# Optimization experiments

Hardware: AMD Instinct MI355X
Metric: run time of the kernel (lower is better)

The kernel has to match this reference:

```python
import jax, jax.numpy as jnp
import numpy as np

N, E, B = 4096, 12288, 64
CLIP, HID, H = 768, 1024, 4
PREFIX, MBART = 4, 768
C2 = PREFIX * MBART
NEG_SLOPE = 0.2


def setup_inputs() -> dict:
    key = jax.random.key(0)
    ks = jax.random.split(key, 30)
    s = 0.05

    def nrm(k, shape, sc=s):
        return jax.random.normal(k, shape, dtype=jnp.float32) * sc

    inp = {
        "x": nrm(ks[0], (N, CLIP), 1.0),
        "edge_index": jax.random.randint(ks[1], (2, E), 0, N),
        "edge_attr": nrm(ks[2], (E, CLIP), 1.0),
        "batch": jnp.sort(jax.random.randint(ks[3], (N,), 0, B)),
        # GATConv 1 (clip_dim -> hidden, H heads, concat=False)
        "W1": nrm(ks[4], (CLIP, H, HID)),
        "att_src1": nrm(ks[5], (H, HID)),
        "att_dst1": nrm(ks[6], (H, HID)),
        "W_edge1": nrm(ks[7], (CLIP, H, HID)),
        "att_edge1": nrm(ks[8], (H, HID)),
        "bias1": jnp.zeros((HID,), jnp.float32),
        "prelu1": jnp.float32(0.25),
        # GATConv 2 (hidden -> prefix*mbart, H heads, concat=False)
        "W2": nrm(ks[9], (HID, H, C2)),
        "att_src2": nrm(ks[10], (H, C2)),
        "att_dst2": nrm(ks[11], (H, C2)),
        "W_edge2": nrm(ks[12], (CLIP, H, C2)),
        "att_edge2": nrm(ks[13], (H, C2)),
        "bias2": jnp.zeros((C2,), jnp.float32),
        "prelu2": jnp.float32(0.25),
        # AttentionalAggregation gate_nn: Linear/PReLU/Linear/PReLU/Linear
        "gW1": nrm(ks[14], (C2, HID)),
        "gb1": jnp.zeros((HID,), jnp.float32),
        "ga1": jnp.float32(0.25),
        "gW2": nrm(ks[15], (HID, HID)),
        "gb2": jnp.zeros((HID,), jnp.float32),
        "ga2": jnp.float32(0.25),
        "gW3": nrm(ks[16], (HID, 1)),
        "gb3": jnp.zeros((1,), jnp.float32),
    }
    return inp


def _prelu(x, a):
    return jnp.where(x >= 0, x, a * x)


def _gat_conv(x, src, dst, edge_attr, W, att_s, att_d, W_e, att_e, bias, n):
    # PyG GATConv, concat=False: shared lin for src/dst, edge-attention term,
    # leaky_relu, segment softmax over destination neighborhoods, scatter-add.
    xl = jnp.einsum('nd,dhc->nhc', x, W)                  # [N,H,C]
    a_s = jnp.einsum('nhc,hc->nh', xl, att_s)             # [N,H]
    a_d = jnp.einsum('nhc,hc->nh', xl, att_d)             # [N,H]
    # fuse lin_edge + att_edge: alpha_e = edge_attr @ (W_e . att_e)
    w_e = jnp.einsum('dhc,hc->dh', W_e, att_e)            # [D_edge,H]
    a_e = edge_attr @ w_e                                 # [E,H]
    alpha = jax.nn.leaky_relu(a_s[src] + a_d[dst] + a_e, NEG_SLOPE)
    # segment softmax grouped by dst
    amax = jax.ops.segment_max(alpha, dst, num_segments=n)
    amax = jnp.where(jnp.isfinite(amax), amax, 0.0)
    ex = jnp.exp(alpha - amax[dst])
    den = jax.ops.segment_sum(ex, dst, num_segments=n)
    coef = ex / (den[dst] + 1e-16)                        # [E,H]
    msg = coef[:, :, None] * xl[src]                      # [E,H,C]
    out = jax.ops.segment_sum(msg, dst, num_segments=n)   # [N,H,C]
    return out.mean(axis=1) + bias                        # concat=False -> head mean


def _forward(x, edge_index, edge_attr, batch,
             W1, att_src1, att_dst1, W_edge1, att_edge1, bias1, prelu1,
             W2, att_src2, att_dst2, W_edge2, att_edge2, bias2, prelu2,
             gW1, gb1, ga1, gW2, gb2, ga2, gW3, gb3):
    n = x.shape[0]
    src, dst = edge_index[0], edge_index[1]
    # add_self_loops with fill_value='mean': self-loop edge_attr = mean of
    # incoming edge_attr per destination node (0 if isolated)
    ones = jnp.ones((src.shape[0],), x.dtype)
    deg = jax.ops.segment_sum(ones, dst, num_segments=n)
    mean_attr = jax.ops.segment_sum(edge_attr, dst, num_segments=n) / jnp.clip(deg, 1.0)[:, None]
    loops = jnp.arange(n)
    src_a = jnp.concatenate([src, loops])
    dst_a = jnp.concatenate([dst, loops])
    ea = jnp.concatenate([edge_attr, mean_attr], axis=0)

    h = _gat_conv(x, src_a, dst_a, ea, W1, att_src1, att_dst1, W_edge1, att_edge1, bias1, n)
    h = _prelu(h, prelu1)
    h = _gat_conv(h, src_a, dst_a, ea, W2, att_src2, att_dst2, W_edge2, att_edge2, bias2, n)
    h = _prelu(h, prelu2)

    # AttentionalAggregation: gate_nn -> segment softmax over batch -> weighted sum
    g = _prelu(h @ gW1 + gb1, ga1)
    g = _prelu(g @ gW2 + gb2, ga2)
    gate = g @ gW3 + gb3                                   # [N,1]
    gmax = jax.ops.segment_max(gate, batch, num_segments=B)
    gmax = jnp.where(jnp.isfinite(gmax), gmax, 0.0)
    eg = jnp.exp(gate - gmax[batch])
    den = jax.ops.segment_sum(eg, batch, num_segments=B)
    coef = eg / (den[batch] + 1e-16)
    pooled = jax.ops.segment_sum(coef * h, batch, num_segments=B)  # [B,C2]
    return pooled.reshape(-1, PREFIX, MBART)


def reference(x, edge_index, edge_attr, batch,
              W1, att_src1, att_dst1, W_edge1, att_edge1, bias1, prelu1,
              W2, att_src2, att_dst2, W_edge2, att_edge2, bias2, prelu2,
              gW1, gb1, ga1, gW2, gb2, ga2, gW3, gb3):
    return _forward(x, edge_index, edge_attr, batch,
                    W1, att_src1, att_dst1, W_edge1, att_edge1, bias1, prelu1,
                    W2, att_src2, att_dst2, W_edge2, att_edge2, bias2, prelu2,
                    gW1, gb1, ga1, gW2, gb2, ga2, gW3, gb3)
```

## Files before the change

kernel.cpp:

```cpp
#include <hip/hip_runtime.h>
#include <stdint.h>
#include <stddef.h>

#define N_NODES  4096
#define N_EDGES  12288
#define EA_EDGES 16384
#define NBATCH   64
#define CLIPD    768
#define HIDD     1024
#define C2D      3072
#define NEG_SLOPE 0.2f
#define MAXDEG   96

typedef unsigned short u16;
typedef short bf16x8 __attribute__((ext_vector_type(8)));
typedef float f32x4  __attribute__((ext_vector_type(4)));

static __device__ __forceinline__ float b2f(u16 u) {
    union { float f; unsigned int i; } v; v.i = ((unsigned int)u) << 16; return v.f;
}
static __device__ __forceinline__ u16 f2b(float f) {
    union { float f; unsigned int i; } v; v.f = f;
    unsigned int r = (v.i + 0x7fffu + ((v.i >> 16) & 1u)) >> 16;
    return (u16)r;
}
static __device__ __forceinline__ void ld4(const float* p, float v[4]) {
    float4 t = *(const float4*)p;
    v[0] = t.x; v[1] = t.y; v[2] = t.z; v[3] = t.w;
}
static __device__ __forceinline__ void ld4(const u16* p, float v[4]) {
    ushort4 t = *(const ushort4*)p;
    v[0] = b2f(t.x); v[1] = b2f(t.y); v[2] = b2f(t.z); v[3] = b2f(t.w);
}

static __device__ __forceinline__ float wsum(float v) {
#pragma unroll
    for (int o = 32; o > 0; o >>= 1) v += __shfl_xor(v, o, 64);
    return v;
}
static __device__ __forceinline__ float wmax(float v) {
#pragma unroll
    for (int o = 32; o > 0; o >>= 1) v = fmaxf(v, __shfl_xor(v, o, 64));
    return v;
}
static __device__ __forceinline__ int lower_bound(const int* a, int n, int key) {
    int lo = 0, hi = n;
    while (lo < hi) { int m = (lo + hi) >> 1; if (a[m] < key) lo = m + 1; else hi = m; }
    return lo;
}

#define GLD16(gp, lp)                                                            \
    __builtin_amdgcn_global_load_lds((const __attribute__((address_space(1))) void*)(gp), \
                                     (__attribute__((address_space(3))) void*)(lp), 16, 0, 0)

__global__ void k_deg(const int* __restrict__ dst, int* __restrict__ deg) {
    int e = blockIdx.x * 256 + threadIdx.x;
    if (e < N_EDGES) atomicAdd(&deg[dst[e]], 1);
}

__global__ void k_scan(const int* __restrict__ deg, int* __restrict__ offs) {
    __shared__ int s[1024];
    int t = threadIdx.x;
    int v[4]; int sum = 0;
#pragma unroll
    for (int i = 0; i < 4; i++) { v[i] = deg[t * 4 + i] + 1; sum += v[i]; }
    s[t] = sum; __syncthreads();
    for (int st = 1; st < 1024; st <<= 1) {
        int x = 0;
        if (t >= st) x = s[t - st];
        __syncthreads();
        s[t] += x;
        __syncthreads();
    }
    int run = s[t] - sum;
#pragma unroll
    for (int i = 0; i < 4; i++) { offs[t * 4 + i] = run; run += v[i]; }
    if (t == 1023) offs[N_NODES] = run;
}

__global__ void k_fill(const int* __restrict__ dst, const int* __restrict__ offs,
                       int* __restrict__ cur, int* __restrict__ csr) {
    int id = blockIdx.x * 256 + threadIdx.x;
    if (id >= EA_EDGES) return;
    int d = (id < N_EDGES) ? dst[id] : (id - N_EDGES);
    int p = atomicAdd(&cur[d], 1);
    csr[offs[d] + p] = id;
}

__global__ void k_reduce_w(const float* __restrict__ W, const float* __restrict__ attA,
                           const float* __restrict__ attB, float* __restrict__ out,
                           int C, int col0) {
    int d = blockIdx.x, t = threadIdx.x;
    float acc[8] = {0, 0, 0, 0, 0, 0, 0, 0};
    for (int c = t * 4; c < C; c += 1024) {
#pragma unroll
        for (int h = 0; h < 4; h++) {
            float4 w = *(const float4*)&W[((size_t)d * 4 + h) * C + c];
            float4 a = *(const float4*)&attA[h * C + c];
            acc[h] += w.x * a.x + w.y * a.y + w.z * a.z + w.w * a.w;
            if (attB) {
                float4 bv = *(const float4*)&attB[h * C + c];
                acc[4 + h] += w.x * bv.x + w.y * bv.y + w.z * bv.z + w.w * bv.w;
            }
        }
    }
    __shared__ float red[4][8];
    int lane = t & 63, wv = t >> 6;
#pragma unroll
    for (int j = 0; j < 8; j++) acc[j] = wsum(acc[j]);
    if (lane == 0) {
#pragma unroll
        for (int j = 0; j < 8; j++) red[wv][j] = acc[j];
    }
    __syncthreads();
    if (t < 8) {
        float s = red[0][t] + red[1][t] + red[2][t] + red[3][t];
        if (attB) out[d * 8 + col0 + t] = s;
        else if (t < 4) out[d * 8 + col0 + t] = s;
    }
}

template <typename T>
__global__ void k_gemv8(const T* __restrict__ X, int K, const float* __restrict__ Wr,
                        float* __restrict__ out, int rows) {
    int wv = threadIdx.x >> 6, lane = threadIdx.x & 63;
    int row = blockIdx.x * 4 + wv;
    if (row >= rows) return;
    float acc[8] = {0, 0, 0, 0, 0, 0, 0, 0};
    const T* xp = X + (size_t)row * K;
    for (int k = lane * 4; k < K; k += 256) {
        float xv[4]; ld4(xp + k, xv);
#pragma unroll
        for (int kk = 0; kk < 4; kk++) {
            const float4* w = (const float4*)(Wr + (size_t)(k + kk) * 8);
            float4 w0 = w[0], w1 = w[1];
            acc[0] += xv[kk] * w0.x; acc[1] += xv[kk] * w0.y;
            acc[2] += xv[kk] * w0.z; acc[3] += xv[kk] * w0.w;
            acc[4] += xv[kk] * w1.x; acc[5] += xv[kk] * w1.y;
            acc[6] += xv[kk] * w1.z; acc[7] += xv[kk] * w1.w;
        }
    }
#pragma unroll
    for (int j = 0; j < 8; j++) acc[j] = wsum(acc[j]);
    if (lane == 0) {
#pragma unroll
        for (int j = 0; j < 8; j++) out[(size_t)row * 8 + j] = acc[j];
    }
}

__global__ void k_selfloop(float* __restrict__ ae, const int* __restrict__ csr,
                           const int* __restrict__ offs, const int* __restrict__ deg) {
    int n = blockIdx.x * 256 + threadIdx.x;
    if (n >= N_NODES) return;
    float s[8] = {0, 0, 0, 0, 0, 0, 0, 0};
    int lo = offs[n], hi = offs[n + 1];
    for (int i = lo; i < hi; i++) {
        int eid = csr[i];
        if (eid < N_EDGES) {
            const float4* p = (const float4*)(ae + (size_t)eid * 8);
            float4 a = p[0], b = p[1];
            s[0] += a.x; s[1] += a.y; s[2] += a.z; s[3] += a.w;
            s[4] += b.x; s[5] += b.y; s[6] += b.z; s[7] += b.w;
        }
    }
    float inv = 1.0f / (float)(deg[n] > 0 ? deg[n] : 1);
    float4* o = (float4*)(ae + (size_t)(N_EDGES + n) * 8);
    float4 o0, o1;
    o0.x = s[0] * inv; o0.y = s[1] * inv; o0.z = s[2] * inv; o0.w = s[3] * inv;
    o1.x = s[4] * inv; o1.y = s[5] * inv; o1.z = s[6] * inv; o1.w = s[7] * inv;
    o[0] = o0; o[1] = o1;
}

template <typename T>
__global__ void k_attn_agg(const T* __restrict__ feat, int D,
                           const float* __restrict__ asd, const float* __restrict__ ae, int aecol,
                           const int* __restrict__ offs, const int* __restrict__ csr,
                           const int* __restrict__ src, u16* __restrict__ agg) {
    int n = blockIdx.x, t = threadIdx.x;
    __shared__ int sl[MAXDEG];
    __shared__ float cf[MAXDEG][4];
    int lo = offs[n];
    int cnt = offs[n + 1] - lo;
    if (cnt > MAXDEG) cnt = MAXDEG;
    for (int i = t; i < cnt; i += 256) {
        int eid = csr[lo + i];
        int s = (eid < N_EDGES) ? src[eid] : n;
        sl[i] = s;
#pragma unroll
        for (int h = 0; h < 4; h++) {
            float al = asd[(size_t)s * 8 + h] + asd[(size_t)n * 8 + 4 + h] +
                       ae[(size_t)eid * 8 + aecol + h];
            cf[i][h] = (al >= 0.f) ? al : NEG_SLOPE * al;
        }
    }
    __syncthreads();
    {
        int wv = t >> 6, lane = t & 63;
        float mx = -1e30f;
        for (int i = lane; i < cnt; i += 64) mx = fmaxf(mx, cf[i][wv]);
        mx = wmax(mx);
        float ds = 0.f;
        for (int i = lane; i < cnt; i += 64) {
            float e = __expf(cf[i][wv] - mx); cf[i][wv] = e; ds += e;
        }
        ds = wsum(ds);
        float inv = 1.0f / (ds + 1e-16f);
        for (int i = lane; i < cnt; i += 64) cf[i][wv] *= inv;
    }
    __syncthreads();
    for (int d4 = t * 4; d4 < D; d4 += 1024) {
        float a[4][4] = {};
        for (int i = 0; i < cnt; i++) {
            float4 c4 = *(const float4*)cf[i];
            float v[4]; ld4(feat + (size_t)sl[i] * D + d4, v);
#pragma unroll
            for (int dj = 0; dj < 4; dj++) {
                a[dj][0] += c4.x * v[dj]; a[dj][1] += c4.y * v[dj];
                a[dj][2] += c4.z * v[dj]; a[dj][3] += c4.w * v[dj];
            }
        }
        u16* op = agg + (size_t)n * 4 * D + (size_t)d4 * 4;
#pragma unroll
        for (int dj = 0; dj < 4; dj++) {
            ushort4 pk;
            pk.x = f2b(a[dj][0]); pk.y = f2b(a[dj][1]);
            pk.z = f2b(a[dj][2]); pk.w = f2b(a[dj][3]);
            *(ushort4*)(op + dj * 4) = pk;
        }
    }
}

__global__ void k_transpose(const float* __restrict__ in, u16* __restrict__ out, int R, int C) {
    __shared__ float tile[64][65];
    int tx = threadIdx.x, ty = threadIdx.y;
    int rb = blockIdx.y * 64, cb = blockIdx.x * 64;
    for (int i = ty; i < 64; i += 4) tile[i][tx] = in[(size_t)(rb + i) * C + cb + tx];
    __syncthreads();
    int linear = ty * 64 + tx;
#pragma unroll
    for (int jj = 0; jj < 4; jj++) {
        int idx = linear + jj * 256;
        int j = idx >> 4, s4 = (idx & 15) * 4;
        ushort4 pk;
        pk.x = f2b(tile[s4 + 0][j]);
        pk.y = f2b(tile[s4 + 1][j]);
        pk.z = f2b(tile[s4 + 2][j]);
        pk.w = f2b(tile[s4 + 3][j]);
        *(ushort4*)(out + (size_t)(cb + j) * R + rb + s4) = pk;
    }
}

template <int BN>
__global__ __launch_bounds__(256, 2) void k_gemm(
        const u16* __restrict__ A, const u16* __restrict__ Bt, void* __restrict__ Cout,
        const float* __restrict__ bias, const float* __restrict__ prelu, float scale,
        int N, int K, int f32out) {
    constexpr int NJ = BN / 32;
    constexpr int NBCH = BN * 8 / 256;
    __shared__ __align__(16) u16 As[128 * 64];
    __shared__ __align__(16) u16 Bs[BN * 64];
    int tid = threadIdx.x;
    int lane = tid & 63, wv = tid >> 6;
    int m0 = blockIdx.y * 128, n0 = blockIdx.x * BN;
    const u16* agp[4]; u16* alp[4];
#pragma unroll
    for (int u = 0; u < 4; u++) {
        int c = tid + u * 256;
        int r = c >> 3, kb = (c & 7) ^ (r & 7);
        agp[u] = A + (size_t)(m0 + r) * K + kb * 8;
        alp[u] = As + c * 8;
    }
    const u16* bgp[NBCH]; u16* blp[NBCH];
#pragma unroll
    for (int u = 0; u < NBCH; u++) {
        int c = tid + u * 256;
        int r = c >> 3, kb = (c & 7) ^ (r & 7);
        bgp[u] = Bt + (size_t)(n0 + r) * K + kb * 8;
        blp[u] = Bs + c * 8;
    }
    int wm = wv & 1, wn = wv >> 1;
    int rl = lane & 15, q = lane >> 4;
    int swz = rl & 7;
    int mb = wm * 64 + rl;
    int nb = wn * (NJ * 16) + rl;
    f32x4 acc[4][NJ] = {};
    for (int k0 = 0; k0 < K; k0 += 64) {
        __syncthreads();
#pragma unroll
        for (int u = 0; u < 4; u++) { GLD16(agp[u], alp[u]); agp[u] += 64; }
#pragma unroll
        for (int u = 0; u < NBCH; u++) { GLD16(bgp[u], blp[u]); bgp[u] += 64; }
        __syncthreads();
        bf16x8 af[4][2], bfr[NJ][2];
#pragma unroll
        for (int i = 0; i < 4; i++)
#pragma unroll
            for (int s = 0; s < 2; s++)
                af[i][s] = *(const bf16x8*)(As + (((mb + i * 16) * 8 + ((q + 4 * s) ^ swz)) * 8));
#pragma unroll
        for (int j = 0; j < NJ; j++)
#pragma unroll
            for (int s = 0; s < 2; s++)
                bfr[j][s] = *(const bf16x8*)(Bs + (((nb + j * 16) * 8 + ((q + 4 * s) ^ swz)) * 8));
#pragma unroll
        for (int i = 0; i < 4; i++)
#pragma unroll
            for (int j = 0; j < NJ; j++) {
                acc[i][j] = __builtin_amdgcn_mfma_f32_16x16x32_bf16(af[i][0], bfr[j][0], acc[i][j], 0, 0, 0);
                acc[i][j] = __builtin_amdgcn_mfma_f32_16x16x32_bf16(af[i][1], bfr[j][1], acc[i][j], 0, 0, 0);
            }
    }
    float pa = prelu[0];
    int r0w = (lane >> 4) * 4;
    int cc = lane & 15;
#pragma unroll
    for (int j = 0; j < NJ; j++) {
        int col = n0 + wn * (NJ * 16) + j * 16 + cc;
        float bv = bias[col];
#pragma unroll
        for (int i = 0; i < 4; i++) {
#pragma unroll
            for (int r = 0; r < 4; r++) {
                int row = m0 + wm * 64 + i * 16 + r0w + r;
                float v = acc[i][j][r] * scale + bv;
                v = (v >= 0.f) ? v : pa * v;
                if (f32out) ((float*)Cout)[(size_t)row * N + col] = v;
                else        ((u16*)Cout)[(size_t)row * N + col] = f2b(v);
            }
        }
    }
}

__global__ void k_gate(const float* __restrict__ g2, const float* __restrict__ gW3,
                       const float* __restrict__ gb3, float* __restrict__ gate) {
    int wv = threadIdx.x >> 6, lane = threadIdx.x & 63;
    int n = blockIdx.x * 4 + wv;
    if (n >= N_NODES) return;
    float s = 0.f;
    const float* gp = g2 + (size_t)n * HIDD;
    for (int k = lane * 4; k < HIDD; k += 256) {
        float4 a = *(const float4*)(gp + k);
        float4 w = *(const float4*)(gW3 + k);
        s += a.x * w.x + a.y * w.y + a.z * w.z + a.w * w.w;
    }
    s = wsum(s);
    if (lane == 0) gate[n] = s + gb3[0];
}

__global__ void k_pool(const float* __restrict__ gate, const u16* __restrict__ h2,
                       const int* __restrict__ batch, float* __restrict__ out) {
    int b = blockIdx.x, t = threadIdx.x;
    int c = blockIdx.y * 1024 + t * 4;
    int lo = lower_bound(batch, N_NODES, b);
    int hi = lower_bound(batch, N_NODES, b + 1);
    int cnt = hi - lo;
    if (cnt <= 0) {
        float4 z; z.x = z.y = z.z = z.w = 0.f;
        *(float4*)(out + (size_t)b * C2D + c) = z;
        return;
    }
    if (cnt > 256) cnt = 256;
    __shared__ float w[256];
    __shared__ float red[4];
    int lane = t & 63, wv = t >> 6;
    float mx = -1e30f;
    for (int i = t; i < cnt; i += 256) mx = fmaxf(mx, gate[lo + i]);
    mx = wmax(mx);
    if (lane == 0) red[wv] = mx;
    __syncthreads();
    mx = fmaxf(fmaxf(red[0], red[1]), fmaxf(red[2], red[3]));
    __syncthreads();
    float ds = 0.f;
    for (int i = t; i < cnt; i += 256) { float e = __expf(gate[lo + i] - mx); w[i] = e; ds += e; }
    ds = wsum(ds);
    if (lane == 0) red[wv] = ds;
    __syncthreads();
    float inv = 1.0f / (red[0] + red[1] + red[2] + red[3] + 1e-16f);
    float4 acc; acc.x = acc.y = acc.z = acc.w = 0.f;
    const u16* hp = h2 + (size_t)lo * C2D + c;
    for (int i = 0; i < cnt; i++) {
        ushort4 hv = *(const ushort4*)hp; hp += C2D;
        float wi = w[i];
        acc.x += wi * b2f(hv.x); acc.y += wi * b2f(hv.y);
        acc.z += wi * b2f(hv.z); acc.w += wi * b2f(hv.w);
    }
    acc.x *= inv; acc.y *= inv; acc.z *= inv; acc.w *= inv;
    *(float4*)(out + (size_t)b * C2D + c) = acc;
}

extern "C" void kernel_launch(void* const* d_in, const int* in_sizes, int n_in,
                              void* d_out, int out_size, void* d_ws, size_t ws_size,
                              hipStream_t stream) {
    (void)in_sizes; (void)n_in; (void)out_size; (void)ws_size;
    const float* x      = (const float*)d_in[0];
    const int*   eidx   = (const int*)d_in[1];
    const float* eattr  = (const float*)d_in[2];
    const int*   batch  = (const int*)d_in[3];
    const float* W1     = (const float*)d_in[4];
    const float* att_s1 = (const float*)d_in[5];
    const float* att_d1 = (const float*)d_in[6];
    const float* We1    = (const float*)d_in[7];
    const float* att_e1 = (const float*)d_in[8];
    const float* bias1  = (const float*)d_in[9];
    const float* prelu1 = (const float*)d_in[10];
    const float* W2     = (const float*)d_in[11];
    const float* att_s2 = (const float*)d_in[12];
    const float* att_d2 = (const float*)d_in[13];
    const float* We2    = (const float*)d_in[14];
    const float* att_e2 = (const float*)d_in[15];
    const float* bias2  = (const float*)d_in[16];
    const float* prelu2 = (const float*)d_in[17];
    const float* gW1    = (const float*)d_in[18];
    const float* gb1    = (const float*)d_in[19];
    const float* ga1    = (const float*)d_in[20];
    const float* gW2    = (const float*)d_in[21];
    const float* gb2    = (const float*)d_in[22];
    const float* ga2    = (const float*)d_in[23];
    const float* gW3    = (const float*)d_in[24];
    const float* gb3    = (const float*)d_in[25];
    const int* srcA = eidx;
    const int* dstA = eidx + N_EDGES;

    char* wp = (char*)d_ws;
    auto alloc = [&](size_t bytes) -> void* {
        void* p = (void*)wp; wp += (bytes + 255) & ~(size_t)255; return p;
    };
    int*   deg  = (int*)alloc(N_NODES * 4);
    int*   cur  = (int*)alloc(N_NODES * 4);
    int*   offs = (int*)alloc((N_NODES + 1) * 4);
    int*   csr  = (int*)alloc(EA_EDGES * 4);
    float* vsd1 = (float*)alloc(CLIPD * 8 * 4);
    float* we12 = (float*)alloc(CLIPD * 8 * 4);
    float* vsd2 = (float*)alloc(HIDD * 8 * 4);
    float* ae   = (float*)alloc((size_t)EA_EDGES * 8 * 4);
    float* asd1 = (float*)alloc((size_t)N_NODES * 8 * 4);
    float* asd2 = (float*)alloc((size_t)N_NODES * 8 * 4);
    float* gate = (float*)alloc(N_NODES * 4);
    char*  aggU = (char*)alloc((size_t)N_NODES * 4096 * 2);
    u16*   agg1 = (u16*)aggU;
    u16*   agg2 = (u16*)aggU;
    float* g2   = (float*)aggU;
    u16*   h1   = (u16*)alloc((size_t)N_NODES * HIDD * 2);
    u16*   g1   = h1;
    u16*   h2   = (u16*)alloc((size_t)N_NODES * C2D * 2);
    u16*   Btb  = (u16*)alloc((size_t)C2D * 4096 * 2);

    hipMemsetAsync(deg, 0, N_NODES * 4, stream);
    hipMemsetAsync(cur, 0, N_NODES * 4, stream);

    k_deg<<<(N_EDGES + 255) / 256, 256, 0, stream>>>(dstA, deg);
    k_scan<<<1, 1024, 0, stream>>>(deg, offs);
    k_fill<<<(EA_EDGES + 255) / 256, 256, 0, stream>>>(dstA, offs, cur, csr);

    k_reduce_w<<<CLIPD, 256, 0, stream>>>(W1, att_s1, att_d1, vsd1, HIDD, 0);
    k_reduce_w<<<CLIPD, 256, 0, stream>>>(We1, att_e1, nullptr, we12, HIDD, 0);
    k_reduce_w<<<HIDD, 256, 0, stream>>>(W2, att_s2, att_d2, vsd2, C2D, 0);
    k_reduce_w<<<CLIPD, 256, 0, stream>>>(We2, att_e2, nullptr, we12, C2D, 4);

    k_gemv8<float><<<N_EDGES / 4, 256, 0, stream>>>(eattr, CLIPD, we12, ae, N_EDGES);
    k_selfloop<<<(N_NODES + 255) / 256, 256, 0, stream>>>(ae, csr, offs, deg);
    k_gemv8<float><<<N_NODES / 4, 256, 0, stream>>>(x, CLIPD, vsd1, asd1, N_NODES);

    k_attn_agg<float><<<N_NODES, 256, 0, stream>>>(x, CLIPD, asd1, ae, 0, offs, csr, srcA, agg1);
    k_transpose<<<dim3(HIDD / 64, C2D / 64), dim3(64, 4), 0, stream>>>(W1, Btb, C2D, HIDD);
    k_gemm<64><<<dim3(HIDD / 64, N_NODES / 128), 256, 0, stream>>>(
        agg1, Btb, h1, bias1, prelu1, 0.25f, HIDD, C2D, 0);

    k_gemv8<u16><<<N_NODES / 4, 256, 0, stream>>>(h1, HIDD, vsd2, asd2, N_NODES);
    k_attn_agg<u16><<<N_NODES, 256, 0, stream>>>(h1, HIDD, asd2, ae, 4, offs, csr, srcA, agg2);
    k_transpose<<<dim3(C2D / 64, 4096 / 64), dim3(64, 4), 0, stream>>>(W2, Btb, 4096, C2D);
    k_gemm<128><<<dim3(C2D / 128, N_NODES / 128), 256, 0, stream>>>(
        agg2, Btb, h2, bias2, prelu2, 0.25f, C2D, 4096, 0);

    k_transpose<<<dim3(HIDD / 64, C2D / 64), dim3(64, 4), 0, stream>>>(gW1, Btb, C2D, HIDD);
    k_gemm<64><<<dim3(HIDD / 64, N_NODES / 128), 256, 0, stream>>>(
        h2, Btb, g1, gb1, ga1, 1.0f, HIDD, C2D, 0);
    k_transpose<<<dim3(HIDD / 64, HIDD / 64), dim3(64, 4), 0, stream>>>(gW2, Btb, HIDD, HIDD);
    k_gemm<64><<<dim3(HIDD / 64, N_NODES / 128), 256, 0, stream>>>(
        g1, Btb, (void*)g2, gb2, ga2, 1.0f, HIDD, HIDD, 1);
    k_gate<<<N_NODES / 4, 256, 0, stream>>>(g2, gW3, gb3, gate);

    k_pool<<<dim3(NBATCH, 3), 256, 0, stream>>>(gate, h2, batch, (float*)d_out);
}
```

Measured before the change: 575.6 us.

## Merge weight-reduce and gemv launches, deepen GEMM K-step, add XCD-aware block remap

Folds the four weight-attention reduction launches into one kernel and the two edge/node gemv launches into a dual-row kernel, cutting launch count and small-kernel tails. The GEMM gains a KSUB template that stages two 64-wide K slices per sync for the BN=64 GEMMs, halving barrier count at the cost of doubled LDS, which may lower occupancy. It also remaps block indices so that consecutive row blocks land on the same XCD, aiming at better L2 reuse of the A tiles.

After: 557.0 us. 1.03x faster.

```diff
diff --git a/kernel.cpp b/kernel.cpp
--- a/kernel.cpp
+++ b/kernel.cpp
@@ -87,10 +87,10 @@
     csr[offs[d] + p] = id;
 }
 
-__global__ void k_reduce_w(const float* __restrict__ W, const float* __restrict__ attA,
-                           const float* __restrict__ attB, float* __restrict__ out,
-                           int C, int col0) {
-    int d = blockIdx.x, t = threadIdx.x;
+static __device__ void reduce_w_body(const float* __restrict__ W, const float* __restrict__ attA,
+                                     const float* __restrict__ attB, float* __restrict__ out,
+                                     int C, int col0, int d) {
+    int t = threadIdx.x;
     float acc[8] = {0, 0, 0, 0, 0, 0, 0, 0};
     for (int c = t * 4; c < C; c += 1024) {
 #pragma unroll
@@ -120,12 +120,24 @@
     }
 }
 
+__global__ void k_reduce_all(const float* __restrict__ W1, const float* __restrict__ as1,
+                             const float* __restrict__ ad1, float* __restrict__ vsd1,
+                             const float* __restrict__ We1, const float* __restrict__ ae1,
+                             const float* __restrict__ W2, const float* __restrict__ as2,
+                             const float* __restrict__ ad2, float* __restrict__ vsd2,
+                             const float* __restrict__ We2, const float* __restrict__ ae2,
+                             float* __restrict__ we12) {
+    int b = blockIdx.x;
+    if (b < CLIPD)                   reduce_w_body(W1, as1, ad1, vsd1, HIDD, 0, b);
+    else if (b < 2 * CLIPD)          reduce_w_body(We1, ae1, nullptr, we12, HIDD, 0, b - CLIPD);
+    else if (b < 2 * CLIPD + HIDD)   reduce_w_body(W2, as2, ad2, vsd2, C2D, 0, b - 2 * CLIPD);
+    else                             reduce_w_body(We2, ae2, nullptr, we12, C2D, 4, b - 2 * CLIPD - HIDD);
+}
+
 template <typename T>
-__global__ void k_gemv8(const T* __restrict__ X, int K, const float* __restrict__ Wr,
-                        float* __restrict__ out, int rows) {
-    int wv = threadIdx.x >> 6, lane = threadIdx.x & 63;
-    int row = blockIdx.x * 4 + wv;
-    if (row >= rows) return;
+static __device__ void gemv8_body(const T* __restrict__ X, int K, const float* __restrict__ Wr,
+                                  float* __restrict__ out, int row) {
+    int lane = threadIdx.x & 63;
     float acc[8] = {0, 0, 0, 0, 0, 0, 0, 0};
     const T* xp = X + (size_t)row * K;
     for (int k = lane * 4; k < K; k += 256) {
@@ -146,6 +158,22 @@
 #pragma unroll
         for (int j = 0; j < 8; j++) out[(size_t)row * 8 + j] = acc[j];
     }
+}
+
+template <typename T>
+__global__ void k_gemv8(const T* __restrict__ X, int K, const float* __restrict__ Wr,
+                        float* __restrict__ out, int rows) {
+    int row = blockIdx.x * 4 + (threadIdx.x >> 6);
+    if (row < rows) gemv8_body(X, K, Wr, out, row);
+}
+
+__global__ void k_gemv8_dual(const float* __restrict__ Xa, const float* __restrict__ Wa,
+                             float* __restrict__ outA, int rowsA,
+                             const float* __restrict__ Xb, const float* __restrict__ Wb,
+                             float* __restrict__ outB) {
+    int row = blockIdx.x * 4 + (threadIdx.x >> 6);
+    if (row < rowsA) gemv8_body(Xa, CLIPD, Wa, outA, row);
+    else             gemv8_body(Xb, CLIPD, Wb, outB, row - rowsA);
 }
 
 __global__ void k_selfloop(float* __restrict__ ae, const int* __restrict__ csr,
@@ -250,33 +278,42 @@
     }
 }
 
-template <int BN>
+template <int BN, int KSUB>
 __global__ __launch_bounds__(256, 2) void k_gemm(
         const u16* __restrict__ A, const u16* __restrict__ Bt, void* __restrict__ Cout,
         const float* __restrict__ bias, const float* __restrict__ prelu, float scale,
         int N, int K, int f32out) {
     constexpr int NJ = BN / 32;
     constexpr int NBCH = BN * 8 / 256;
-    __shared__ __align__(16) u16 As[128 * 64];
-    __shared__ __align__(16) u16 Bs[BN * 64];
+    __shared__ __align__(16) u16 As[KSUB * 128 * 64];
+    __shared__ __align__(16) u16 Bs[KSUB * BN * 64];
     int tid = threadIdx.x;
     int lane = tid & 63, wv = tid >> 6;
-    int m0 = blockIdx.y * 128, n0 = blockIdx.x * BN;
-    const u16* agp[4]; u16* alp[4];
+    int gx = gridDim.x;
+    int bx = blockIdx.x, by = blockIdx.y;
+    if ((gx & 7) == 0) {
+        int flat = by * gx + bx;
+        int nx_per = gx >> 3;
+        int xcd = flat & 7, idx = flat >> 3;
+        bx = xcd * nx_per + idx % nx_per;
+        by = idx / nx_per;
+    }
+    int m0 = by * 128, n0 = bx * BN;
+    const u16* agp[4]; int alo[4];
 #pragma unroll
     for (int u = 0; u < 4; u++) {
         int c = tid + u * 256;
         int r = c >> 3, kb = (c & 7) ^ (r & 7);
         agp[u] = A + (size_t)(m0 + r) * K + kb * 8;
-        alp[u] = As + c * 8;
-    }
-    const u16* bgp[NBCH]; u16* blp[NBCH];
+        alo[u] = c * 8;
+    }
+    const u16* bgp[NBCH]; int blo[NBCH];
 #pragma unroll
     for (int u = 0; u < NBCH; u++) {
         int c = tid + u * 256;
         int r = c >> 3, kb = (c & 7) ^ (r & 7);
         bgp[u] = Bt + (size_t)(n0 + r) * K + kb * 8;
-        blp[u] = Bs + c * 8;
+        blo[u] = c * 8;
     }
     int wm = wv & 1, wn = wv >> 1;
     int rl = lane & 15, q = lane >> 4;
@@ -284,31 +321,43 @@
     int mb = wm * 64 + rl;
     int nb = wn * (NJ * 16) + rl;
     f32x4 acc[4][NJ] = {};
-    for (int k0 = 0; k0 < K; k0 += 64) {
+    for (int k0 = 0; k0 < K; k0 += 64 * KSUB) {
         __syncthreads();
 #pragma unroll
-        for (int u = 0; u < 4; u++) { GLD16(agp[u], alp[u]); agp[u] += 64; }
-#pragma unroll
-        for (int u = 0; u < NBCH; u++) { GLD16(bgp[u], blp[u]); bgp[u] += 64; }
+        for (int su = 0; su < KSUB; su++) {
+#pragma unroll
+            for (int u = 0; u < 4; u++)    GLD16(agp[u] + su * 64, As + su * (128 * 64) + alo[u]);
+#pragma unroll
+            for (int u = 0; u < NBCH; u++) GLD16(bgp[u] + su * 64, Bs + su * (BN * 64) + blo[u]);
+        }
+#pragma unroll
+        for (int u = 0; u < 4; u++)    agp[u] += 64 * KSUB;
+#pragma unroll
+        for (int u = 0; u < NBCH; u++) bgp[u] += 64 * KSUB;
         __syncthreads();
-        bf16x8 af[4][2], bfr[NJ][2];
-#pragma unroll
-        for (int i = 0; i < 4; i++)
-#pragma unroll
-            for (int s = 0; s < 2; s++)
-                af[i][s] = *(const bf16x8*)(As + (((mb + i * 16) * 8 + ((q + 4 * s) ^ swz)) * 8));
-#pragma unroll
-        for (int j = 0; j < NJ; j++)
-#pragma unroll
-            for (int s = 0; s < 2; s++)
-                bfr[j][s] = *(const bf16x8*)(Bs + (((nb + j * 16) * 8 + ((q + 4 * s) ^ swz)) * 8));
-#pragma unroll
-        for (int i = 0; i < 4; i++)
-#pragma unroll
-            for (int j = 0; j < NJ; j++) {
-                acc[i][j] = __builtin_amdgcn_mfma_f32_16x16x32_bf16(af[i][0], bfr[j][0], acc[i][j], 0, 0, 0);
-                acc[i][j] = __builtin_amdgcn_mfma_f32_16x16x32_bf16(af[i][1], bfr[j][1], acc[i][j], 0, 0, 0);
-            }
+#pragma unroll
+        for (int su = 0; su < KSUB; su++) {
+            const u16* Asb = As + su * (128 * 64);
+            const u16* Bsb = Bs + su * (BN * 64);
+            bf16x8 af[4][2], bfr[NJ][2];
+#pragma unroll
+            for (int i = 0; i < 4; i++)
+#pragma unroll
+                for (int s = 0; s < 2; s++)
+                    af[i][s] = *(const bf16x8*)(Asb + (((mb + i * 16) * 8 + ((q + 4 * s) ^ swz)) * 8));
+#pragma unroll
+            for (int j = 0; j < NJ; j++)
+#pragma unroll
+                for (int s = 0; s < 2; s++)
+                    bfr[j][s] = *(const bf16x8*)(Bsb + (((nb + j * 16) * 8 + ((q + 4 * s) ^ swz)) * 8));
+#pragma unroll
+            for (int i = 0; i < 4; i++)
+#pragma unroll
+                for (int j = 0; j < NJ; j++) {
+                    acc[i][j] = __builtin_amdgcn_mfma_f32_16x16x32_bf16(af[i][0], bfr[j][0], acc[i][j], 0, 0, 0);
+                    acc[i][j] = __builtin_amdgcn_mfma_f32_16x16x32_bf16(af[i][1], bfr[j][1], acc[i][j], 0, 0, 0);
+                }
+        }
     }
     float pa = prelu[0];
     int r0w = (lane >> 4) * 4;
@@ -452,31 +501,29 @@
     k_scan<<<1, 1024, 0, stream>>>(deg, offs);
     k_fill<<<(EA_EDGES + 255) / 256, 256, 0, stream>>>(dstA, offs, cur, csr);
 
-    k_reduce_w<<<CLIPD, 256, 0, stream>>>(W1, att_s1, att_d1, vsd1, HIDD, 0);
-    k_reduce_w<<<CLIPD, 256, 0, stream>>>(We1, att_e1, nullptr, we12, HIDD, 0);
-    k_reduce_w<<<HIDD, 256, 0, stream>>>(W2, att_s2, att_d2, vsd2, C2D, 0);
-    k_reduce_w<<<CLIPD, 256, 0, stream>>>(We2, att_e2, nullptr, we12, C2D, 4);
-
-    k_gemv8<float><<<N_EDGES / 4, 256, 0, stream>>>(eattr, CLIPD, we12, ae, N_EDGES);
+    k_reduce_all<<<2 * CLIPD + HIDD + CLIPD, 256, 0, stream>>>(
+        W1, att_s1, att_d1, vsd1, We1, att_e1, W2, att_s2, att_d2, vsd2, We2, att_e2, we12);
+
+    k_gemv8_dual<<<(N_EDGES + N_NODES) / 4, 256, 0, stream>>>(
+        eattr, we12, ae, N_EDGES, x, vsd1, asd1);
     k_selfloop<<<(N_NODES + 255) / 256, 256, 0, stream>>>(ae, csr, offs, deg);
-    k_gemv8<float><<<N_NODES / 4, 256, 0, stream>>>(x, CLIPD, vsd1, asd1, N_NODES);
 
     k_attn_agg<float><<<N_NODES, 256, 0, stream>>>(x, CLIPD, asd1, ae, 0, offs, csr, srcA, agg1);
     k_transpose<<<dim3(HIDD / 64, C2D / 64), dim3(64, 4), 0, stream>>>(W1, Btb, C2D, HIDD);
-    k_gemm<64><<<dim3(HIDD / 64, N_NODES / 128), 256, 0, stream>>>(
+    k_gemm<64, 2><<<dim3(HIDD / 64, N_NODES / 128), 256, 0, stream>>>(
         agg1, Btb, h1, bias1, prelu1, 0.25f, HIDD, C2D, 0);
 
     k_gemv8<u16><<<N_NODES / 4, 256, 0, stream>>>(h1, HIDD, vsd2, asd2, N_NODES);
     k_attn_agg<u16><<<N_NODES, 256, 0, stream>>>(h1, HIDD, asd2, ae, 4, offs, csr, srcA, agg2);
     k_transpose<<<dim3(C2D / 64, 4096 / 64), dim3(64, 4), 0, stream>>>(W2, Btb, 4096, C2D);
-    k_gemm<128><<<dim3(C2D / 128, N_NODES / 128), 256, 0, stream>>>(
+    k_gemm<128, 1><<<dim3(C2D / 128, N_NODES / 128), 256, 0, stream>>>(
         agg2, Btb, h2, bias2, prelu2, 0.25f, C2D, 4096, 0);
 
     k_transpose<<<dim3(HIDD / 64, C2D / 64), dim3(64, 4), 0, stream>>>(gW1, Btb, C2D, HIDD);
-    k_gemm<64><<<dim3(HIDD / 64, N_NODES / 128), 256, 0, stream>>>(
+    k_gemm<64, 2><<<dim3(HIDD / 64, N_NODES / 128), 256, 0, stream>>>(
         h2, Btb, g1, gb1, ga1, 1.0f, HIDD, C2D, 0);
     k_transpose<<<dim3(HIDD / 64, HIDD / 64), dim3(64, 4), 0, stream>>>(gW2, Btb, HIDD, HIDD);
-    k_gemm<64><<<dim3(HIDD / 64, N_NODES / 128), 256, 0, stream>>>(
+    k_gemm<64, 2><<<dim3(HIDD / 64, N_NODES / 128), 256, 0, stream>>>(
         g1, Btb, (void*)g2, gb2, ga2, 1.0f, HIDD, HIDD, 1);
     k_gate<<<N_NODES / 4, 256, 0, stream>>>(g2, gW3, gb3, gate);
 
```
